# Kernel tuning notes

Hardware: AMD Instinct MI355X
Metric: run time of the kernel (lower is better)

Reference implementation:

```python
import jax, jax.numpy as jnp
import numpy as np

EPS = 1e-5

def splice(x, offsets):
    # x: [B, F, T]; offsets already shifted so offsets[0] == 0.
    # Output channel order matches torch reshape(-1, C*F): y[b, f*C+c, t] = x[b, f, t+off[c]]
    w = offsets[-1]
    Tn = x.shape[2] - w
    y = jnp.stack([x[:, :, o:o + Tn] for o in offsets], axis=2)  # [B, F, C, Tn]
    B, F, C, _ = y.shape
    return y.reshape(B, F * C, Tn)

def conv1x1(x, w, b):
    # x: [B, Cin, T], w: [Cout, Cin], b: [Cout]
    return jnp.einsum('oc,bct->bot', w, x) + b[None, :, None]

def bn_ct(x, gamma=None, beta=None):
    # BatchNorm1d (training mode, biased var) over (batch, time) per channel
    m = x.mean(axis=(0, 2), keepdims=True)
    v = x.var(axis=(0, 2), keepdims=True)
    y = (x - m) * jax.lax.rsqrt(v + EPS)
    if gamma is not None:
        y = y * gamma[None, :, None] + beta[None, :, None]
    return y

def bn_c(x, gamma, beta):
    # BatchNorm1d on [B, C]
    m = x.mean(axis=0, keepdims=True)
    v = x.var(axis=0, keepdims=True)
    return (x - m) * jax.lax.rsqrt(v + EPS) * gamma[None, :] + beta[None, :]

def relu6(x):
    return jnp.clip(x, 0.0, 6.0)

def setup_inputs() -> dict:
    key = jax.random.key(0)
    ks = list(jax.random.split(key, 32))
    def rn(shape, scale=0.05):
        return jax.random.normal(ks.pop(), shape, dtype=jnp.float32) * scale
    inp = {
        'x': jax.random.normal(ks.pop(), (32, 2048, 20), dtype=jnp.float32),
        'h1_w': rn((512, 100)), 'h1_b': rn((512,)),
        'h2_w': rn((512, 1536)), 'h2_b': rn((512,)),
        'bn2_g': jnp.ones((512,), jnp.float32), 'bn2_b': jnp.zeros((512,), jnp.float32),
        'h3_w': rn((512, 1536)), 'h3_b': rn((512,)),
        'bn3_g': jnp.ones((512,), jnp.float32), 'bn3_b': jnp.zeros((512,), jnp.float32),
        'h4_w': rn((512, 512)), 'h4_b': rn((512,)),
        'bn4_g': jnp.ones((512,), jnp.float32), 'bn4_b': jnp.zeros((512,), jnp.float32),
        'h5_w': rn((1500, 512)), 'h5_b': rn((1500,)),
        'bn5_g': jnp.ones((1500,), jnp.float32), 'bn5_b': jnp.zeros((1500,), jnp.float32),
        'l1_w': rn((512, 3000)), 'l1_b': rn((512,)),
        'bn6_g': jnp.ones((512,), jnp.float32), 'bn6_b': jnp.zeros((512,), jnp.float32),
        'l2_w': rn((512, 512)), 'l2_b': rn((512,)),
        'bn7_g': jnp.ones((512,), jnp.float32), 'bn7_b': jnp.zeros((512,), jnp.float32),
    }
    return inp

def reference(x, h1_w, h1_b, h2_w, h2_b, bn2_g, bn2_b, h3_w, h3_b, bn3_g, bn3_b,
              h4_w, h4_b, bn4_g, bn4_b, h5_w, h5_b, bn5_g, bn5_b,
              l1_w, l1_b, bn6_g, bn6_b, l2_w, l2_b, bn7_g, bn7_b):
    o = jnp.transpose(x, (0, 2, 1))                     # [B, 20, T]
    o = splice(o, (0, 1, 2, 3, 4))                      # context [-2..2] -> [B, 100, T-4]
    o = bn_ct(jax.nn.relu(conv1x1(o, h1_w, h1_b)))      # bn1 affine=False
    o = splice(o, (0, 2, 4))                            # context [-2,0,2] -> [B, 1536, T-8]
    o = bn_ct(jax.nn.relu(conv1x1(o, h2_w, h2_b)), bn2_g, bn2_b)
    o = splice(o, (0, 3, 6))                            # context [-3,0,3] -> [B, 1536, T-14]
    o = bn_ct(jax.nn.relu(conv1x1(o, h3_w, h3_b)), bn3_g, bn3_b)
    o = bn_ct(relu6(conv1x1(o, h4_w, h4_b)), bn4_g, bn4_b)
    o = bn_ct(relu6(conv1x1(o, h5_w, h5_b)), bn5_g, bn5_b)  # [B, 1500, T']
    mean = o.mean(axis=-1)
    std = jnp.std(o, axis=-1, ddof=1)                   # torch.std is unbiased
    o = jnp.concatenate((mean, std), axis=1)            # [B, 3000]
    o = bn_c(relu6(o @ l1_w.T + l1_b), bn6_g, bn6_b)
    o = bn_c(relu6(o @ l2_w.T + l2_b), bn7_g, bn7_b)
    return o
```

## Files before the change

kernel.cpp:

```cpp
#include <hip/hip_runtime.h>
#include <cstdint>

#define EPSF 1e-5f

namespace {

typedef _Float16 f16;
typedef _Float16 v8h __attribute__((ext_vector_type(8)));
typedef float v4f __attribute__((ext_vector_type(4)));

constexpr int B  = 32;
constexpr int T0 = 2048, F0 = 20;
constexpr int T1 = 2044, T2 = 2040, T3 = 2034;
constexpr int TS = 2048;

__device__ __forceinline__ void gload16(const void* g, void* l) {
    typedef const __attribute__((address_space(1))) void* gp_t;
    typedef __attribute__((address_space(3))) void* lp_t;
    __builtin_amdgcn_global_load_lds((gp_t)(unsigned long long)g,
                                     (lp_t)(unsigned int)(unsigned long long)l,
                                     16, 0, 0);
}
__device__ __forceinline__ void wait_vm4() { asm volatile("s_waitcnt vmcnt(4)" ::: "memory"); }
__device__ __forceinline__ void wait_vm0() { asm volatile("s_waitcnt vmcnt(0)" ::: "memory"); }

__global__ __launch_bounds__(256) void transpose_x(const float* __restrict__ x,
                                                   f16* __restrict__ xT,
                                                   float* __restrict__ stZ)
{
    int idx = blockIdx.x * 256 + threadIdx.x;
    if (idx < 4096) stZ[idx] = 0.f;
    constexpr int total = B * 3 * TS * 8;
    if (idx >= total) return;
    int fl = idx & 7;
    int t  = (idx >> 3) & (TS - 1);
    int fo = (idx >> 14) % 3;
    int b  = idx / (3 << 14);
    int f  = fo * 8 + fl;
    float v = (f < F0) ? x[((size_t)b * T0 + t) * F0 + f] : 0.f;
    xT[idx] = (f16)v;
}

template<int FP, int C>
__global__ __launch_bounds__(256) void fold_mfma(
    const float* __restrict__ W, const float* __restrict__ bias,
    const float* __restrict__ st, const float* __restrict__ gamma, const float* __restrict__ beta,
    f16* __restrict__ Wh, float* __restrict__ bf,
    int Oreal, int Freal, int Cin, int CinOrig, float invN)
{
    int o = blockIdx.x;
    auto sidx = [&](int k) {
        return ((size_t)((o >> 7) * (Cin >> 3) + (k >> 3)) * 128 + (o & 127)) * 8 + (k & 7);
    };
    if (o >= Oreal) {
        for (int k = threadIdx.x; k < Cin; k += 256) Wh[sidx(k)] = (f16)0.f;
        if (threadIdx.x == 0) bf[o] = 0.f;
        return;
    }
    float local = 0.f;
    for (int k = threadIdx.x; k < Cin; k += 256) {
        int c = k / FP, f = k - c * FP;
        float wv = 0.f;
        if (c < C && f < Freal) {
            float sc = 1.f, sh = 0.f;
            if (st) {
                float mean = st[f] * invN;
                float var  = st[Freal + f] * invN - mean * mean;
                sc = rsqrtf(var + EPSF);
                if (gamma) sc *= gamma[f];
                sh = (beta ? beta[f] : 0.f) - mean * sc;
            }
            float w = W[(size_t)o * CinOrig + f * C + c];
            wv = w * sc;
            local += w * sh;
        }
        Wh[sidx(k)] = (f16)wv;
    }
#pragma unroll
    for (int d = 32; d; d >>= 1) local += __shfl_down(local, d);
    __shared__ float red[4];
    if ((threadIdx.x & 63) == 0) red[threadIdx.x >> 6] = local;
    __syncthreads();
    if (threadIdx.x == 0) bf[o] = bias[o] + red[0] + red[1] + red[2] + red[3];
}

template<int ACT, int FPR, int CIN>
__global__ __launch_bounds__(256, 4) void conv_mfma(
    const f16* __restrict__ inT, const f16* __restrict__ Wh,
    const float* __restrict__ bias, f16* __restrict__ outT,
    float* __restrict__ st, int O, int Tout, int offMul)
{
    __shared__ __align__(16) f16 Ilds[2][4 * 128 * 8];
    __shared__ __align__(16) f16 Wlds[2][4 * 128 * 8];
    __shared__ float redS[2][128];
    __shared__ float redQ[2][128];
    const int tid  = threadIdx.x;
    const int lane = tid & 63, wave = tid >> 6;
    const int wt = wave & 1, wo = wave >> 1;
    const int quad = lane >> 4, l16 = lane & 15;
    const int tB = blockIdx.x * 128, oB = blockIdx.y * 128, b = blockIdx.z;
    const f16* inb = inT + (size_t)b * FPR * TS;
    const size_t wBase = (size_t)(oB >> 7) * (CIN >> 3);

    auto stage = [&](int iB, int pb) {
#pragma unroll
        for (int j = 0; j < 4; ++j) {
            int s = wave * 4 + j;
            int koct = (s & 7) >> 1, half = s & 1;
            if (s < 8) {
                int kidx = iB + koct * 8;
                int c = kidx / FPR, f = kidx - c * FPR;
                int t = tB + half * 64 + lane + c * offMul;
                gload16(inb + ((size_t)(f >> 3) * TS + t) * 8,
                        &Ilds[pb][(koct * 128 + half * 64) * 8]);
            } else {
                gload16(Wh + ((wBase + (iB >> 3) + koct) * 128 + half * 64 + lane) * 8,
                        &Wlds[pb][(koct * 128 + half * 64) * 8]);
            }
        }
    };

    v4f acc[4][4];
#pragma unroll
    for (int mi = 0; mi < 4; ++mi)
#pragma unroll
        for (int ni = 0; ni < 4; ++ni)
#pragma unroll
            for (int r = 0; r < 4; ++r) acc[mi][ni][r] = 0.f;

    constexpr int nIter = CIN >> 5;
    stage(0, 0);
#pragma unroll 2
    for (int k = 0; k < nIter; ++k) {
        const int pb = k & 1;
        __syncthreads();
        if (k + 1 < nIter) { stage((k + 1) * 32, pb ^ 1); wait_vm4(); }
        else               { wait_vm0(); }
        __syncthreads();
        v8h afr[4], bfr[4];
#pragma unroll
        for (int mi = 0; mi < 4; ++mi)
            afr[mi] = *(const v8h*)&Ilds[pb][(quad * 128 + wt * 64 + mi * 16 + l16) * 8];
#pragma unroll
        for (int ni = 0; ni < 4; ++ni)
            bfr[ni] = *(const v8h*)&Wlds[pb][(quad * 128 + wo * 64 + ni * 16 + l16) * 8];
#pragma unroll
        for (int mi = 0; mi < 4; ++mi)
#pragma unroll
            for (int ni = 0; ni < 4; ++ni)
                acc[mi][ni] = __builtin_amdgcn_mfma_f32_16x16x32_f16(
                    afr[mi], bfr[ni], acc[mi][ni], 0, 0, 0);
    }

    float Sl[4] = {0, 0, 0, 0}, Ql[4] = {0, 0, 0, 0};
#pragma unroll
    for (int ni = 0; ni < 4; ++ni) {
        const int o  = oB + wo * 64 + ni * 16 + l16;
        const float bs = bias[o];
        f16* orow = outT + (size_t)b * O * TS + (size_t)(o >> 3) * TS * 8 + (o & 7);
#pragma unroll
        for (int mi = 0; mi < 4; ++mi)
#pragma unroll
            for (int r = 0; r < 4; ++r) {
                int t = tB + wt * 64 + mi * 16 + quad * 4 + r;
                if (t < Tout) {
                    float v = acc[mi][ni][r] + bs;
                    v = fmaxf(v, 0.f);
                    if (ACT == 2) v = fminf(v, 6.f);
                    orow[(size_t)t * 8] = (f16)v;
                    Sl[ni] += v; Ql[ni] += v * v;
                }
            }
    }
#pragma unroll
    for (int ni = 0; ni < 4; ++ni) {
        float s = Sl[ni], q = Ql[ni];
        s += __shfl_down(s, 32); q += __shfl_down(q, 32);
        s += __shfl_down(s, 16); q += __shfl_down(q, 16);
        if (lane < 16) {
            redS[wt][wo * 64 + ni * 16 + lane] = s;
            redQ[wt][wo * 64 + ni * 16 + lane] = q;
        }
    }
    __syncthreads();
    if (tid < 128) {
        atomicAdd(&st[oB + tid],       redS[0][tid] + redS[1][tid]);
        atomicAdd(&st[512 + oB + tid], redQ[0][tid] + redQ[1][tid]);
    }
}

template<int CIN>
__global__ __launch_bounds__(256, 4) void pool_mfma(
    const f16* __restrict__ inT, const f16* __restrict__ Wh,
    const float* __restrict__ bias, float* __restrict__ Sp, float* __restrict__ Qp,
    int T, int Opad)
{
    const int L    = blockIdx.x;
    const int slot = L >> 3;
    const int oB   = (slot % 12) * 128;
    const int cz   = (L & 7) + 8 * (slot / 12);
    const int b    = cz & 31, z = cz >> 5;

    __shared__ __align__(16) f16 Ilds[2][4 * 128 * 8];
    __shared__ __align__(16) f16 Wlds[2][4 * 128 * 8];
    __shared__ float redS[2][128];
    __shared__ float redQ[2][128];
    const int tid  = threadIdx.x;
    const int lane = tid & 63, wave = tid >> 6;
    const int wt = wave & 1, wo = wave >> 1;
    const int quad = lane >> 4, l16 = lane & 15;
    const f16* inb = inT + (size_t)b * CIN * TS;
    const size_t wBase = (size_t)(oB >> 7) * (CIN >> 3);

    auto stage = [&](int t0, int iB, int pb) {
#pragma unroll
        for (int j = 0; j < 4; ++j) {
            int s = wave * 4 + j;
            int koct = (s & 7) >> 1, half = s & 1;
            if (s < 8) {
                gload16(inb + ((size_t)((iB >> 3) + koct) * TS + t0 + half * 64 + lane) * 8,
                        &Ilds[pb][(koct * 128 + half * 64) * 8]);
            } else {
                gload16(Wh + ((wBase + (iB >> 3) + koct) * 128 + half * 64 + lane) * 8,
                        &Wlds[pb][(koct * 128 + half * 64) * 8]);
            }
        }
    };

    float Sl[4] = {0, 0, 0, 0}, Ql[4] = {0, 0, 0, 0};
    float bs[4];
#pragma unroll
    for (int ni = 0; ni < 4; ++ni) bs[ni] = bias[oB + wo * 64 + ni * 16 + l16];

    const int tBase = z * 512;
    constexpr int kPer  = CIN >> 5;
    constexpr int total = 4 * kPer;

    v4f acc[4][4];
#pragma unroll
    for (int mi = 0; mi < 4; ++mi)
#pragma unroll
        for (int ni = 0; ni < 4; ++ni)
#pragma unroll
            for (int r = 0; r < 4; ++r) acc[mi][ni][r] = 0.f;

    stage(tBase, 0, 0);
#pragma unroll 2
    for (int it = 0; it < total; ++it) {
        const int pb = it & 1;
        __syncthreads();
        if (it + 1 < total) {
            int nx = it + 1;
            stage(tBase + (nx >> 4) * 128, (nx & (kPer - 1)) * 32, pb ^ 1);
            wait_vm4();
        } else {
            wait_vm0();
        }
        __syncthreads();
        v8h afr[4], bfr[4];
#pragma unroll
        for (int mi = 0; mi < 4; ++mi)
            afr[mi] = *(const v8h*)&Ilds[pb][(quad * 128 + wt * 64 + mi * 16 + l16) * 8];
#pragma unroll
        for (int ni = 0; ni < 4; ++ni)
            bfr[ni] = *(const v8h*)&Wlds[pb][(quad * 128 + wo * 64 + ni * 16 + l16) * 8];
#pragma unroll
        for (int mi = 0; mi < 4; ++mi)
#pragma unroll
            for (int ni = 0; ni < 4; ++ni)
                acc[mi][ni] = __builtin_amdgcn_mfma_f32_16x16x32_f16(
                    afr[mi], bfr[ni], acc[mi][ni], 0, 0, 0);

        if ((it & (kPer - 1)) == kPer - 1) {
            int tB = tBase + (it >> 4) * 128;
#pragma unroll
            for (int ni = 0; ni < 4; ++ni)
#pragma unroll
                for (int mi = 0; mi < 4; ++mi)
#pragma unroll
                    for (int r = 0; r < 4; ++r) {
                        int t = tB + wt * 64 + mi * 16 + quad * 4 + r;
                        if (t < T) {
                            float v = fminf(fmaxf(acc[mi][ni][r] + bs[ni], 0.f), 6.f);
                            Sl[ni] += v; Ql[ni] += v * v;
                        }
                        acc[mi][ni][r] = 0.f;
                    }
        }
    }

#pragma unroll
    for (int ni = 0; ni < 4; ++ni) {
        float s = Sl[ni], q = Ql[ni];
        s += __shfl_down(s, 32); q += __shfl_down(q, 32);
        s += __shfl_down(s, 16); q += __shfl_down(q, 16);
        if (lane < 16) {
            redS[wt][wo * 64 + ni * 16 + lane] = s;
            redQ[wt][wo * 64 + ni * 16 + lane] = q;
        }
    }
    __syncthreads();
    if (tid < 128) {
        int o = oB + tid;
        Sp[((size_t)z * B + b) * Opad + o] = redS[0][tid] + redS[1][tid];
        Qp[((size_t)z * B + b) * Opad + o] = redQ[0][tid] + redQ[1][tid];
    }
}

__global__ __launch_bounds__(256) void pool_finalize(
    const float* __restrict__ Sp, const float* __restrict__ Qp,
    const float* __restrict__ g5, const float* __restrict__ b5,
    float* __restrict__ stat, int Opad, int Oreal, int T)
{
    int co = blockIdx.x * 256 + threadIdx.x;
    if (co >= Oreal) return;
    double sS = 0, sQ = 0;
    for (int z = 0; z < 4; ++z)
        for (int b = 0; b < B; ++b) {
            sS += Sp[((size_t)z * B + b) * Opad + co];
            sQ += Qp[((size_t)z * B + b) * Opad + co];
        }
    double invN = 1.0 / ((double)B * T);
    double m = sS * invN;
    double v = sQ * invN - m * m;
    float sc = g5[co] * rsqrtf((float)v + EPSF);
    float sh = b5[co] - (float)m * sc;
    for (int b = 0; b < B; ++b) {
        double sb = 0, qb = 0;
        for (int z = 0; z < 4; ++z) {
            sb += Sp[((size_t)z * B + b) * Opad + co];
            qb += Qp[((size_t)z * B + b) * Opad + co];
        }
        double mb = sb / T;
        double vb = (qb - sb * sb / T) / (T - 1);
        if (vb < 0) vb = 0;
        stat[(size_t)b * 2 * Oreal + co]         = (float)mb * sc + sh;
        stat[(size_t)b * 2 * Oreal + Oreal + co] = sqrtf((float)vb) * fabsf(sc);
    }
}

__global__ __launch_bounds__(256) void fc_relu6(const float* __restrict__ x,
                                                const float* __restrict__ W,
                                                const float* __restrict__ bias,
                                                float* __restrict__ y, int Cin, int O)
{
    int wid = (blockIdx.x * 256 + threadIdx.x) >> 6;
    int lane = threadIdx.x & 63;
    if (wid >= B * O) return;
    int b = wid / O, o = wid - b * O;
    const float* xr = x + (size_t)b * Cin;
    const float* wr = W + (size_t)o * Cin;
    float s = 0.f;
    for (int c = lane; c < Cin; c += 64) s = fmaf(xr[c], wr[c], s);
#pragma unroll
    for (int d = 32; d; d >>= 1) s += __shfl_down(s, d);
    if (lane == 0) y[wid] = fminf(fmaxf(s + bias[o], 0.f), 6.f);
}

__global__ __launch_bounds__(512) void bn_batch(const float* __restrict__ x,
                                                const float* __restrict__ g,
                                                const float* __restrict__ be,
                                                float* __restrict__ y, int O)
{
    int o = threadIdx.x;
    if (o >= O) return;
    float s = 0.f, q = 0.f;
    for (int b = 0; b < B; ++b) { float v = x[b * O + o]; s += v; q += v * v; }
    float m = s / B;
    float var = q / B - m * m;
    float sc = g[o] * rsqrtf(var + EPSF);
    float sh = be[o] - m * sc;
    for (int b = 0; b < B; ++b) y[b * O + o] = x[b * O + o] * sc + sh;
}

}

extern "C" void kernel_launch(void* const* d_in, const int* in_sizes, int n_in,
                              void* d_out, int out_size, void* d_ws, size_t ws_size,
                              hipStream_t stream)
{
    (void)in_sizes; (void)n_in; (void)out_size; (void)ws_size;
    const float* x     = (const float*)d_in[0];
    const float* h1_w  = (const float*)d_in[1];
    const float* h1_b  = (const float*)d_in[2];
    const float* h2_w  = (const float*)d_in[3];
    const float* h2_b  = (const float*)d_in[4];
    const float* bn2_g = (const float*)d_in[5];
    const float* bn2_b = (const float*)d_in[6];
    const float* h3_w  = (const float*)d_in[7];
    const float* h3_b  = (const float*)d_in[8];
    const float* bn3_g = (const float*)d_in[9];
    const float* bn3_b = (const float*)d_in[10];
    const float* h4_w  = (const float*)d_in[11];
    const float* h4_b  = (const float*)d_in[12];
    const float* bn4_g = (const float*)d_in[13];
    const float* bn4_b = (const float*)d_in[14];
    const float* h5_w  = (const float*)d_in[15];
    const float* h5_b  = (const float*)d_in[16];
    const float* bn5_g = (const float*)d_in[17];
    const float* bn5_b = (const float*)d_in[18];
    const float* l1_w  = (const float*)d_in[19];
    const float* l1_b  = (const float*)d_in[20];
    const float* bn6_g = (const float*)d_in[21];
    const float* bn6_b = (const float*)d_in[22];
    const float* l2_w  = (const float*)d_in[23];
    const float* l2_b  = (const float*)d_in[24];
    const float* bn7_g = (const float*)d_in[25];
    const float* bn7_b = (const float*)d_in[26];

    char* ws = (char*)d_ws;
    size_t off = 0;
    auto alloc = [&](size_t bytes) {
        char* p = ws + off;
        off += (bytes + 255) & ~(size_t)255;
        return (void*)p;
    };
    f16* xT    = (f16*)alloc(((size_t)B * 3  * TS * 8 + 2048) * 2);
    f16* bufA  = (f16*)alloc(((size_t)B * 64 * TS * 8 + 2048) * 2);
    f16* bufB  = (f16*)alloc(((size_t)B * 64 * TS * 8 + 2048) * 2);
    f16* Wh1   = (f16*)alloc((size_t)512 * 128 * 2);
    f16* Wh2   = (f16*)alloc((size_t)512 * 1536 * 2);
    f16* Wh3   = (f16*)alloc((size_t)512 * 1536 * 2);
    f16* Wh4   = (f16*)alloc((size_t)512 * 512 * 2);
    f16* Wh5   = (f16*)alloc((size_t)1536 * 512 * 2);
    float* bf1 = (float*)alloc(512 * 4);
    float* bf2 = (float*)alloc(512 * 4);
    float* bf3 = (float*)alloc(512 * 4);
    float* bf4 = (float*)alloc(512 * 4);
    float* bf5 = (float*)alloc(1536 * 4);
    float* stZ = (float*)alloc(4096 * 4);
    float* st1 = stZ, *st2 = stZ + 1024, *st3 = stZ + 2048, *st4 = stZ + 3072;
    float* Sp  = (float*)alloc((size_t)4 * B * 1536 * 4);
    float* Qp  = (float*)alloc((size_t)4 * B * 1536 * 4);
    float* stat = (float*)alloc((size_t)B * 3000 * 4);
    float* f1  = (float*)alloc((size_t)B * 512 * 4);
    float* f2  = (float*)alloc((size_t)B * 512 * 4);

    transpose_x<<<(B * 3 * TS * 8 + 255) / 256, 256, 0, stream>>>(x, xT, stZ);

    fold_mfma<24, 5><<<512, 256, 0, stream>>>(h1_w, h1_b, nullptr, nullptr, nullptr,
                                              Wh1, bf1, 512, 20, 128, 100, 0.f);
    conv_mfma<1, 24, 128><<<dim3(16, 4, B), 256, 0, stream>>>(
        xT, Wh1, bf1, bufA, st1, 512, T1, 1);

    fold_mfma<512, 3><<<512, 256, 0, stream>>>(h2_w, h2_b, st1, nullptr, nullptr,
                                               Wh2, bf2, 512, 512, 1536, 1536,
                                               1.f / (B * T1));
    conv_mfma<1, 512, 1536><<<dim3(16, 4, B), 256, 0, stream>>>(
        bufA, Wh2, bf2, bufB, st2, 512, T2, 2);

    fold_mfma<512, 3><<<512, 256, 0, stream>>>(h3_w, h3_b, st2, bn2_g, bn2_b,
                                               Wh3, bf3, 512, 512, 1536, 1536,
                                               1.f / (B * T2));
    conv_mfma<1, 512, 1536><<<dim3(16, 4, B), 256, 0, stream>>>(
        bufB, Wh3, bf3, bufA, st3, 512, T3, 3);

    fold_mfma<512, 1><<<512, 256, 0, stream>>>(h4_w, h4_b, st3, bn3_g, bn3_b,
                                               Wh4, bf4, 512, 512, 512, 512,
                                               1.f / (B * T3));
    conv_mfma<2, 512, 512><<<dim3(16, 4, B), 256, 0, stream>>>(
        bufA, Wh4, bf4, bufB, st4, 512, T3, 0);

    fold_mfma<512, 1><<<1536, 256, 0, stream>>>(h5_w, h5_b, st4, bn4_g, bn4_b,
                                                Wh5, bf5, 1500, 512, 512, 512,
                                                1.f / (B * T3));
    pool_mfma<512><<<1536, 256, 0, stream>>>(bufB, Wh5, bf5, Sp, Qp, T3, 1536);

    pool_finalize<<<6, 256, 0, stream>>>(Sp, Qp, bn5_g, bn5_b, stat, 1536, 1500, T3);

    fc_relu6<<<(B * 512 * 64 + 255) / 256, 256, 0, stream>>>(stat, l1_w, l1_b, f1, 3000, 512);
    bn_batch<<<1, 512, 0, stream>>>(f1, bn6_g, bn6_b, f1, 512);
    fc_relu6<<<(B * 512 * 64 + 255) / 256, 256, 0, stream>>>(f1, l2_w, l2_b, f2, 512, 512);
    bn_batch<<<1, 512, 0, stream>>>(f2, bn7_g, bn7_b, (float*)d_out, 512);
}
```

Before: 689.6 us.

## Load weight fragments directly to registers, bypassing LDS, in 512-input conv and pool

```diff
diff --git a/kernel.cpp b/kernel.cpp
--- a/kernel.cpp
+++ b/kernel.cpp
@@ -22,6 +22,7 @@
                                      16, 0, 0);
 }
 __device__ __forceinline__ void wait_vm4() { asm volatile("s_waitcnt vmcnt(4)" ::: "memory"); }
+__device__ __forceinline__ void wait_vm6() { asm volatile("s_waitcnt vmcnt(6)" ::: "memory"); }
 __device__ __forceinline__ void wait_vm0() { asm volatile("s_waitcnt vmcnt(0)" ::: "memory"); }
 
 __global__ __launch_bounds__(256) void transpose_x(const float* __restrict__ x,
@@ -91,7 +92,7 @@
     float* __restrict__ st, int O, int Tout, int offMul)
 {
     __shared__ __align__(16) f16 Ilds[2][4 * 128 * 8];
-    __shared__ __align__(16) f16 Wlds[2][4 * 128 * 8];
+    __shared__ __align__(16) f16 Wlds[(FPR == 512) ? 8 : (2 * 4 * 128 * 8)];
     __shared__ float redS[2][128];
     __shared__ float redQ[2][128];
     const int tid  = threadIdx.x;
@@ -102,54 +103,98 @@
     const f16* inb = inT + (size_t)b * FPR * TS;
     const size_t wBase = (size_t)(oB >> 7) * (CIN >> 3);
 
-    auto stage = [&](int iB, int pb) {
-#pragma unroll
-        for (int j = 0; j < 4; ++j) {
-            int s = wave * 4 + j;
-            int koct = (s & 7) >> 1, half = s & 1;
-            if (s < 8) {
-                int kidx = iB + koct * 8;
-                int c = kidx / FPR, f = kidx - c * FPR;
-                int t = tB + half * 64 + lane + c * offMul;
-                gload16(inb + ((size_t)(f >> 3) * TS + t) * 8,
-                        &Ilds[pb][(koct * 128 + half * 64) * 8]);
-            } else {
-                gload16(Wh + ((wBase + (iB >> 3) + koct) * 128 + half * 64 + lane) * 8,
-                        &Wlds[pb][(koct * 128 + half * 64) * 8]);
+    v4f acc[4][4];
+#pragma unroll
+    for (int mi = 0; mi < 4; ++mi)
+#pragma unroll
+        for (int ni = 0; ni < 4; ++ni)
+#pragma unroll
+            for (int r = 0; r < 4; ++r) acc[mi][ni][r] = 0.f;
+
+    constexpr int nIter = CIN >> 5;
+
+    if constexpr (FPR == 512) {
+        const char* gpI = (const char*)(inb + ((size_t)wave * TS + tB + lane) * 8);
+        const char* gpW = (const char*)Wh + ((wBase + quad) * 128 + wo * 64 + l16) * 16;
+        const intptr_t dNI  = (intptr_t)4 * TS * 16;
+        const intptr_t dWrI = ((intptr_t)(-60) * TS + offMul) * 16;
+        v8h wreg[2][4];
+
+        auto prefetch = [&](int pb) {
+#pragma unroll
+            for (int ni = 0; ni < 4; ++ni)
+                wreg[pb][ni] = *(const v8h*)(gpW + ni * 256);
+            f16* Ib = &Ilds[pb][0];
+            gload16(gpI,        Ib + (wave * 128) * 8);
+            gload16(gpI + 1024, Ib + (wave * 128 + 64) * 8);
+        };
+        auto advance = [&](int kFrom) {
+            bool wrap = ((kFrom + 1) & 15) == 0;
+            gpI += wrap ? dWrI : dNI;
+            gpW += 8192;
+        };
+
+        prefetch(0);
+        advance(0);
+#pragma unroll 2
+        for (int k = 0; k < nIter; ++k) {
+            const int pb = k & 1;
+            __syncthreads();
+            if (k + 1 < nIter) { prefetch(pb ^ 1); advance(k + 1); wait_vm6(); }
+            else               { wait_vm0(); }
+            __syncthreads();
+            v8h afr[4];
+#pragma unroll
+            for (int mi = 0; mi < 4; ++mi)
+                afr[mi] = *(const v8h*)&Ilds[pb][(quad * 128 + wt * 64 + mi * 16 + l16) * 8];
+#pragma unroll
+            for (int mi = 0; mi < 4; ++mi)
+#pragma unroll
+                for (int ni = 0; ni < 4; ++ni)
+                    acc[mi][ni] = __builtin_amdgcn_mfma_f32_16x16x32_f16(
+                        afr[mi], wreg[pb][ni], acc[mi][ni], 0, 0, 0);
+        }
+    } else {
+        auto stage = [&](int iB, int pb) {
+#pragma unroll
+            for (int j = 0; j < 4; ++j) {
+                int s = wave * 4 + j;
+                int koct = (s & 7) >> 1, half = s & 1;
+                if (s < 8) {
+                    int kidx = iB + koct * 8;
+                    int c = kidx / FPR, f = kidx - c * FPR;
+                    int t = tB + half * 64 + lane + c * offMul;
+                    gload16(inb + ((size_t)(f >> 3) * TS + t) * 8,
+                            &Ilds[pb][(koct * 128 + half * 64) * 8]);
+                } else {
+                    gload16(Wh + ((wBase + (iB >> 3) + koct) * 128 + half * 64 + lane) * 8,
+                            &Wlds[pb * 4 * 128 * 8 + (koct * 128 + half * 64) * 8]);
+                }
             }
-        }
-    };
-
-    v4f acc[4][4];
-#pragma unroll
-    for (int mi = 0; mi < 4; ++mi)
-#pragma unroll
-        for (int ni = 0; ni < 4; ++ni)
-#pragma unroll
-            for (int r = 0; r < 4; ++r) acc[mi][ni][r] = 0.f;
-
-    constexpr int nIter = CIN >> 5;
-    stage(0, 0);
+        };
+        stage(0, 0);
 #pragma unroll 2
-    for (int k = 0; k < nIter; ++k) {
-        const int pb = k & 1;
-        __syncthreads();
-        if (k + 1 < nIter) { stage((k + 1) * 32, pb ^ 1); wait_vm4(); }
-        else               { wait_vm0(); }
-        __syncthreads();
-        v8h afr[4], bfr[4];
-#pragma unroll
-        for (int mi = 0; mi < 4; ++mi)
-            afr[mi] = *(const v8h*)&Ilds[pb][(quad * 128 + wt * 64 + mi * 16 + l16) * 8];
-#pragma unroll
-        for (int ni = 0; ni < 4; ++ni)
-            bfr[ni] = *(const v8h*)&Wlds[pb][(quad * 128 + wo * 64 + ni * 16 + l16) * 8];
-#pragma unroll
-        for (int mi = 0; mi < 4; ++mi)
+        for (int k = 0; k < nIter; ++k) {
+            const int pb = k & 1;
+            __syncthreads();
+            if (k + 1 < nIter) { stage((k + 1) * 32, pb ^ 1); wait_vm4(); }
+            else               { wait_vm0(); }
+            __syncthreads();
+            v8h afr[4], bfr[4];
+#pragma unroll
+            for (int mi = 0; mi < 4; ++mi)
+                afr[mi] = *(const v8h*)&Ilds[pb][(quad * 128 + wt * 64 + mi * 16 + l16) * 8];
 #pragma unroll
             for (int ni = 0; ni < 4; ++ni)
-                acc[mi][ni] = __builtin_amdgcn_mfma_f32_16x16x32_f16(
-                    afr[mi], bfr[ni], acc[mi][ni], 0, 0, 0);
+                bfr[ni] = *(const v8h*)&Wlds[pb * 4 * 128 * 8 +
+                                             (quad * 128 + wo * 64 + ni * 16 + l16) * 8];
+#pragma unroll
+            for (int mi = 0; mi < 4; ++mi)
+#pragma unroll
+                for (int ni = 0; ni < 4; ++ni)
+                    acc[mi][ni] = __builtin_amdgcn_mfma_f32_16x16x32_f16(
+                        afr[mi], bfr[ni], acc[mi][ni], 0, 0, 0);
+        }
     }
 
     float Sl[4] = {0, 0, 0, 0}, Ql[4] = {0, 0, 0, 0};
@@ -202,7 +247,6 @@
     const int b    = cz & 31, z = cz >> 5;
 
     __shared__ __align__(16) f16 Ilds[2][4 * 128 * 8];
-    __shared__ __align__(16) f16 Wlds[2][4 * 128 * 8];
     __shared__ float redS[2][128];
     __shared__ float redQ[2][128];
     const int tid  = threadIdx.x;
@@ -212,21 +256,6 @@
     const f16* inb = inT + (size_t)b * CIN * TS;
     const size_t wBase = (size_t)(oB >> 7) * (CIN >> 3);
 
-    auto stage = [&](int t0, int iB, int pb) {
-#pragma unroll
-        for (int j = 0; j < 4; ++j) {
-            int s = wave * 4 + j;
-            int koct = (s & 7) >> 1, half = s & 1;
-            if (s < 8) {
-                gload16(inb + ((size_t)((iB >> 3) + koct) * TS + t0 + half * 64 + lane) * 8,
-                        &Ilds[pb][(koct * 128 + half * 64) * 8]);
-            } else {
-                gload16(Wh + ((wBase + (iB >> 3) + koct) * 128 + half * 64 + lane) * 8,
-                        &Wlds[pb][(koct * 128 + half * 64) * 8]);
-            }
-        }
-    };
-
     float Sl[4] = {0, 0, 0, 0}, Ql[4] = {0, 0, 0, 0};
     float bs[4];
 #pragma unroll
@@ -244,32 +273,46 @@
 #pragma unroll
             for (int r = 0; r < 4; ++r) acc[mi][ni][r] = 0.f;
 
-    stage(tBase, 0, 0);
+    const char* gpI = (const char*)(inb + ((size_t)wave * TS + tBase + lane) * 8);
+    const char* gpW = (const char*)Wh + ((wBase + quad) * 128 + wo * 64 + l16) * 16;
+    const intptr_t dNI  = (intptr_t)4 * TS * 16;
+    const intptr_t dWrI = ((intptr_t)(-60) * TS + 128) * 16;
+    const intptr_t dWrW = (intptr_t)(-60) * 2048;
+    v8h wreg[2][4];
+
+    auto prefetch = [&](int pb) {
+#pragma unroll
+        for (int ni = 0; ni < 4; ++ni)
+            wreg[pb][ni] = *(const v8h*)(gpW + ni * 256);
+        f16* Ib = &Ilds[pb][0];
+        gload16(gpI,        Ib + (wave * 128) * 8);
+        gload16(gpI + 1024, Ib + (wave * 128 + 64) * 8);
+    };
+    auto advance = [&](int itFrom) {
+        bool wrap = ((itFrom + 1) & 15) == 0;
+        gpI += wrap ? dWrI : dNI;
+        gpW += wrap ? dWrW : (intptr_t)8192;
+    };
+
+    prefetch(0);
+    advance(0);
 #pragma unroll 2
     for (int it = 0; it < total; ++it) {
         const int pb = it & 1;
         __syncthreads();
-        if (it + 1 < total) {
-            int nx = it + 1;
-            stage(tBase + (nx >> 4) * 128, (nx & (kPer - 1)) * 32, pb ^ 1);
-            wait_vm4();
-        } else {
-            wait_vm0();
-        }
+        if (it + 1 < total) { prefetch(pb ^ 1); advance(it + 1); wait_vm6(); }
+        else                { wait_vm0(); }
         __syncthreads();
-        v8h afr[4], bfr[4];
+        v8h afr[4];
 #pragma unroll
         for (int mi = 0; mi < 4; ++mi)
             afr[mi] = *(const v8h*)&Ilds[pb][(quad * 128 + wt * 64 + mi * 16 + l16) * 8];
 #pragma unroll
-        for (int ni = 0; ni < 4; ++ni)
-            bfr[ni] = *(const v8h*)&Wlds[pb][(quad * 128 + wo * 64 + ni * 16 + l16) * 8];
-#pragma unroll
         for (int mi = 0; mi < 4; ++mi)
 #pragma unroll
             for (int ni = 0; ni < 4; ++ni)
                 acc[mi][ni] = __builtin_amdgcn_mfma_f32_16x16x32_f16(
-                    afr[mi], bfr[ni], acc[mi][ni], 0, 0, 0);
+                    afr[mi], wreg[pb][ni], acc[mi][ni], 0, 0, 0);
 
         if ((it & (kPer - 1)) == kPer - 1) {
             int tB = tBase + (it >> 4) * 128;
```

After: 779.9 us. 1.13x slower.
